# Kernel tuning notes

Measured on AMD Instinct MI355X. Metric: run time of the kernel, lower is better.

## Reference

```python
import jax, jax.numpy as jnp
import numpy as np

FILTER_SIZE = 9
WIN_NUMEL = FILTER_SIZE ** 3  # 729
EPS = 1e-06


def _conv3d_valid(x, w):
    # x: [N,1,D,H,W], w: [1,1,k,k,k]; valid padding, stride 1 (matches F.conv3d padding=0)
    return jax.lax.conv_general_dilated(
        x, w, window_strides=(1, 1, 1), padding='VALID',
        dimension_numbers=('NCDHW', 'OIDHW', 'NCDHW'))


def setup_inputs() -> dict:
    key = jax.random.key(0)
    k1, k2 = jax.random.split(key)
    shape = (1, 1, 160, 160, 160)
    I = jax.random.uniform(k1, shape, dtype=jnp.float32)
    J = jax.random.uniform(k2, shape, dtype=jnp.float32)
    filt = jnp.ones((1, 1, FILTER_SIZE, FILTER_SIZE, FILTER_SIZE), dtype=jnp.float32)
    return {'I': I, 'J': J, 'filt': filt}


def reference(I, J, filt):
    I_sum = _conv3d_valid(I, filt)
    J_sum = _conv3d_valid(J, filt)
    I2_sum = _conv3d_valid(I * I, filt)
    J2_sum = _conv3d_valid(J * J, filt)
    IJ_sum = _conv3d_valid(I * J, filt)

    I_mean = I_sum / WIN_NUMEL
    J_mean = J_sum / WIN_NUMEL

    cross = IJ_sum - I_mean * J_sum - J_mean * I_sum + I_mean * J_mean * WIN_NUMEL
    I_var = I2_sum - 2.0 * I_mean * I_sum + (I_mean ** 2) * WIN_NUMEL
    J_var = J2_sum - 2.0 * J_mean * J_sum + (J_mean ** 2) * WIN_NUMEL

    cc = (cross ** 2) / (I_var * J_var + EPS)
    return 1.0 - jnp.mean(cc)
```

## Files before the change

kernel.cpp:

```cpp
#include <hip/hip_runtime.h>

#define NN 160
#define MM 152
#define TO 16
#define TI 24
#define PSTR 24
#define PCH  (TI*PSTR)
#define XROW 28
#define XCH  (TO*XROW)
#define YROW 20
#define YCH  (TO*YROW)
#define ZC 19
#define PL (ZC+8)
#define KMAX (PL+2)
#define NZ 8
#define NTX 10
#define NTILE 100
#define NBLK (NTILE*8)
#define INV_WIN (1.0f/729.0f)

#define STEP_BARRIER() asm volatile("s_waitcnt lgkmcnt(0)\n\ts_barrier" ::: "memory")

__device__ __forceinline__ float cc_of(const float* s) {
    float cross = fmaf(-s[0] * s[1], INV_WIN, s[4]);
    float iv    = fmaf(-s[0] * s[0], INV_WIN, s[2]);
    float jv    = fmaf(-s[1] * s[1], INV_WIN, s[3]);
    return (cross * cross) / (iv * jv + 1e-6f);
}

__global__ __launch_bounds__(256, 4) void lncc_fused(
    const float* __restrict__ I, const float* __restrict__ J,
    float* __restrict__ partial)
{
    __shared__ float Pld[2][2 * PCH];
    __shared__ float xsb[2][5 * XCH];
    __shared__ float ysb[2][5 * YCH];
    __shared__ float red[4];

    const int tid  = threadIdx.x;
    const int orig = blockIdx.x;
    const int bid  = (orig & 7) * NTILE + (orig >> 3);
    const int tile = bid % NTILE;
    const int zc   = bid / NTILE;
    const int x0 = (tile % NTX) * TO;
    const int y0 = (tile / NTX) * TO;
    const int z0 = zc * ZC;

    const int yl = tid >> 4, xl = tid & 15;
    const bool valid = (x0 + xl < MM) && (y0 + yl < MM);

    const int lrow = tid / 6;
    const int lq   = tid - 6 * lrow;
    const int gy   = min(y0 + lrow, NN - 1);
    const int gx   = min(x0 + lq * 4, NN - 4);
    const size_t pbase = (size_t)gy * NN + gx;

    const int rowX = tid >> 2;
    const int xbX  = (tid & 3) * 4;

    const int eY = tid - 96;
    const int cY = eY >> 4;
    const int xY = eY & 15;

    float4 pI, pJ;
    if (tid < 144) {
        size_t a = (size_t)z0 * (NN * NN) + pbase;
        pI = *(const float4*)(I + a);
        pJ = *(const float4*)(J + a);
    }

    float ring[9][5];
    float sz[5] = {0.f, 0.f, 0.f, 0.f, 0.f};
    float cc_acc = 0.f;

    for (int kb = 0; kb <= KMAX; kb += 9) {
#pragma unroll
        for (int ki = 0; ki < 9; ++ki) {
            const int k = kb + ki;
            if (k > KMAX) continue;

            if (k <= PL - 1 && tid < 144) {
                float* P = &Pld[k & 1][0];
                *(float4*)&P[lrow * PSTR + lq * 4]       = pI;
                *(float4*)&P[PCH + lrow * PSTR + lq * 4] = pJ;
                if (k <= PL - 2) {
                    size_t adr = (size_t)(z0 + k + 1) * (NN * NN) + pbase;
                    pI = *(const float4*)(I + adr);
                    pJ = *(const float4*)(J + adr);
                }
            }

            if (k >= 1 && k <= PL && tid < 96) {
                const int b = (k - 1) & 1;
                const float* P = &Pld[b][0];
                const float4* Ir = (const float4*)&P[rowX * PSTR + xbX];
                const float4* Jr = (const float4*)&P[PCH + rowX * PSTR + xbX];
                float4 i0 = Ir[0], i1 = Ir[1], i2 = Ir[2];
                float4 j0 = Jr[0], j1 = Jr[1], j2 = Jr[2];
                float iv[12], jv[12];
                iv[0]=i0.x; iv[1]=i0.y; iv[2]=i0.z; iv[3]=i0.w;
                iv[4]=i1.x; iv[5]=i1.y; iv[6]=i1.z; iv[7]=i1.w;
                iv[8]=i2.x; iv[9]=i2.y; iv[10]=i2.z; iv[11]=i2.w;
                jv[0]=j0.x; jv[1]=j0.y; jv[2]=j0.z; jv[3]=j0.w;
                jv[4]=j1.x; jv[5]=j1.y; jv[6]=j1.z; jv[7]=j1.w;
                jv[8]=j2.x; jv[9]=j2.y; jv[10]=j2.z; jv[11]=j2.w;
#pragma unroll
                for (int c = 0; c < 5; ++c) {
                    float m[12];
#pragma unroll
                    for (int t = 0; t < 12; ++t) {
                        float av = (c & 1) ? jv[t] : iv[t];
                        float bv = (c < 2) ? 1.0f : ((c == 2) ? iv[t] : jv[t]);
                        m[t] = av * bv;
                    }
                    float s = m[0]+m[1]+m[2]+m[3]+m[4]+m[5]+m[6]+m[7]+m[8];
                    float* W = &xsb[b][c * XCH + rowX];
                    W[xbX * XROW] = s;
#pragma unroll
                    for (int t = 1; t < 4; ++t) {
                        s += m[t + 8] - m[t - 1];
                        W[(xbX + t) * XROW] = s;
                    }
                }
            }

            if (k >= 2 && k <= PL + 1 && tid >= 96 && tid < 176) {
                const int b = (k - 2) & 1;
                const float4* R = (const float4*)&xsb[b][cY * XCH + xY * XROW];
                float4 w0 = R[0], w1 = R[1], w2 = R[2], w3 = R[3], w4 = R[4], w5 = R[5];
                float m[24];
                m[0]=w0.x;  m[1]=w0.y;  m[2]=w0.z;  m[3]=w0.w;
                m[4]=w1.x;  m[5]=w1.y;  m[6]=w1.z;  m[7]=w1.w;
                m[8]=w2.x;  m[9]=w2.y;  m[10]=w2.z; m[11]=w2.w;
                m[12]=w3.x; m[13]=w3.y; m[14]=w3.z; m[15]=w3.w;
                m[16]=w4.x; m[17]=w4.y; m[18]=w4.z; m[19]=w4.w;
                m[20]=w5.x; m[21]=w5.y; m[22]=w5.z; m[23]=w5.w;
                float o[16];
                float s = m[0]+m[1]+m[2]+m[3]+m[4]+m[5]+m[6]+m[7]+m[8];
                o[0] = s;
#pragma unroll
                for (int t = 1; t < 16; ++t) {
                    s += m[t + 8] - m[t - 1];
                    o[t] = s;
                }
                float4* Wv = (float4*)&ysb[b][cY * YCH + xY * YROW];
                float4 oa = {o[0],  o[1],  o[2],  o[3]};
                float4 ob = {o[4],  o[5],  o[6],  o[7]};
                float4 oc = {o[8],  o[9],  o[10], o[11]};
                float4 od = {o[12], o[13], o[14], o[15]};
                Wv[0] = oa; Wv[1] = ob; Wv[2] = oc; Wv[3] = od;
            }

            if (k >= 3) {
                const int b = (k - 3) & 1;
                const int slot  = (ki + 6) % 9;
                const int slot2 = (ki + 7) % 9;
                float v[5];
#pragma unroll
                for (int c = 0; c < 5; ++c) {
                    v[c] = ysb[b][c * YCH + xl * YROW + yl];
                    sz[c] += v[c];
                    ring[slot][c] = v[c];
                }
                if (k >= 11) {
                    cc_acc += valid ? cc_of(sz) : 0.f;
#pragma unroll
                    for (int c = 0; c < 5; ++c) sz[c] -= ring[slot2][c];
                }
            }

            STEP_BARRIER();
        }
    }

    for (int off = 32; off > 0; off >>= 1)
        cc_acc += __shfl_down(cc_acc, off, 64);
    if ((tid & 63) == 0) red[tid >> 6] = cc_acc;
    __syncthreads();
    if (tid == 0) partial[orig] = red[0] + red[1] + red[2] + red[3];
}

__global__ __launch_bounds__(256) void lncc_final(
    const float* __restrict__ partial, float* __restrict__ out)
{
    double s = 0.0;
    for (int i = threadIdx.x; i < NBLK; i += 256)
        s += (double)partial[i];
    for (int off = 32; off > 0; off >>= 1)
        s += __shfl_down(s, off, 64);
    __shared__ double red[4];
    const int lane = threadIdx.x & 63, wid = threadIdx.x >> 6;
    if (lane == 0) red[wid] = s;
    __syncthreads();
    if (threadIdx.x == 0) {
        double tot = red[0] + red[1] + red[2] + red[3];
        out[0] = (float)(1.0 - tot / ((double)MM * MM * MM));
    }
}

extern "C" void kernel_launch(void* const* d_in, const int* in_sizes, int n_in,
                              void* d_out, int out_size, void* d_ws, size_t ws_size,
                              hipStream_t stream) {
    const float* I = (const float*)d_in[0];
    const float* J = (const float*)d_in[1];

    float* partial = (float*)d_ws;

    lncc_fused<<<NBLK, 256, 0, stream>>>(I, J, partial);
    lncc_final<<<1,    256, 0, stream>>>(partial, (float*)d_out);
    (void)in_sizes; (void)n_in; (void)out_size; (void)ws_size;
}
```

Before: 38.67 us.

## Reshape tiles to 8x32 and rebalance warp roles across load, x and y passes

Changes the per-block output tile from 16x16 to 8 wide by 32 tall, which makes the x-direction halo cover an exact 152-wide grid (19 tiles, no invalid x columns) and changes the halo overhead ratio. Reassigns thread roles so that 80 threads do the x-pass, 80 threads load two float4 pairs each, and 80 threads do the y-pass, so that stages no longer sit on overlapping warps and wave-level divergence drops. The cost is a larger y halo (40 rows loaded for 32 outputs) and different LDS strides, which may bring bank conflicts.

```diff
diff --git a/kernel.cpp b/kernel.cpp
--- a/kernel.cpp
+++ b/kernel.cpp
@@ -2,20 +2,21 @@
 
 #define NN 160
 #define MM 152
-#define TO 16
-#define TI 24
-#define PSTR 24
-#define PCH  (TI*PSTR)
-#define XROW 28
-#define XCH  (TO*XROW)
-#define YROW 20
-#define YCH  (TO*YROW)
+#define TOX 8
+#define TOY 32
+#define TIX 16
+#define TIY 40
+#define PS  20
+#define PCH (TIY*PS)
+#define XST 44
+#define XCH (TOX*XST)
+#define YST 36
+#define YCH (TOX*YST)
 #define ZC 19
-#define PL (ZC+8)
-#define KMAX (PL+2)
-#define NZ 8
-#define NTX 10
-#define NTILE 100
+#define PL 27
+#define KMAX 29
+#define NTX 19
+#define NTILE 95
 #define NBLK (NTILE*8)
 #define INV_WIN (1.0f/729.0f)
 
@@ -42,31 +43,34 @@
     const int bid  = (orig & 7) * NTILE + (orig >> 3);
     const int tile = bid % NTILE;
     const int zc   = bid / NTILE;
-    const int x0 = (tile % NTX) * TO;
-    const int y0 = (tile / NTX) * TO;
+    const int x0 = (tile % NTX) * TOX;
+    const int y0 = (tile / NTX) * TOY;
     const int z0 = zc * ZC;
 
-    const int yl = tid >> 4, xl = tid & 15;
-    const bool valid = (x0 + xl < MM) && (y0 + yl < MM);
-
-    const int lrow = tid / 6;
-    const int lq   = tid - 6 * lrow;
-    const int gy   = min(y0 + lrow, NN - 1);
-    const int gx   = min(x0 + lq * 4, NN - 4);
-    const size_t pbase = (size_t)gy * NN + gx;
-
-    const int rowX = tid >> 2;
-    const int xbX  = (tid & 3) * 4;
-
-    const int eY = tid - 96;
-    const int cY = eY >> 4;
-    const int xY = eY & 15;
-
-    float4 pI, pJ;
-    if (tid < 144) {
-        size_t a = (size_t)z0 * (NN * NN) + pbase;
-        pI = *(const float4*)(I + a);
-        pJ = *(const float4*)(J + a);
+    const int yl = tid >> 3, xl = tid & 7;
+    const bool valid = (y0 + yl < MM);
+
+    const int rowX = tid >> 1;
+    const int qX   = tid & 1;
+
+    const int ce = tid - 80;
+    const int r0 = ce >> 2,        q0 = ce & 3;
+    const int r1 = (ce + 80) >> 2, q1 = (ce + 80) & 3;
+    const size_t gb0 = (size_t)min(y0 + r0, NN - 1) * NN + (x0 + q0 * 4);
+    const size_t gb1 = (size_t)min(y0 + r1, NN - 1) * NN + (x0 + q1 * 4);
+
+    const int eY  = tid - 176;
+    const int cY  = eY >> 4;
+    const int xY  = (eY >> 1) & 7;
+    const int yhY = eY & 1;
+
+    float4 pI0, pJ0, pI1, pJ1;
+    if (tid >= 80 && tid < 160) {
+        const size_t zb = (size_t)z0 * (NN * NN);
+        pI0 = *(const float4*)(I + zb + gb0);
+        pJ0 = *(const float4*)(J + zb + gb0);
+        pI1 = *(const float4*)(I + zb + gb1);
+        pJ1 = *(const float4*)(J + zb + gb1);
     }
 
     float ring[9][5];
@@ -79,22 +83,26 @@
             const int k = kb + ki;
             if (k > KMAX) continue;
 
-            if (k <= PL - 1 && tid < 144) {
+            if (k <= PL - 1 && tid >= 80 && tid < 160) {
                 float* P = &Pld[k & 1][0];
-                *(float4*)&P[lrow * PSTR + lq * 4]       = pI;
-                *(float4*)&P[PCH + lrow * PSTR + lq * 4] = pJ;
+                *(float4*)&P[r0 * PS + q0 * 4]       = pI0;
+                *(float4*)&P[PCH + r0 * PS + q0 * 4] = pJ0;
+                *(float4*)&P[r1 * PS + q1 * 4]       = pI1;
+                *(float4*)&P[PCH + r1 * PS + q1 * 4] = pJ1;
                 if (k <= PL - 2) {
-                    size_t adr = (size_t)(z0 + k + 1) * (NN * NN) + pbase;
-                    pI = *(const float4*)(I + adr);
-                    pJ = *(const float4*)(J + adr);
-                }
-            }
-
-            if (k >= 1 && k <= PL && tid < 96) {
+                    const size_t zb = (size_t)(z0 + k + 1) * (NN * NN);
+                    pI0 = *(const float4*)(I + zb + gb0);
+                    pJ0 = *(const float4*)(J + zb + gb0);
+                    pI1 = *(const float4*)(I + zb + gb1);
+                    pJ1 = *(const float4*)(J + zb + gb1);
+                }
+            }
+
+            if (k >= 1 && k <= PL && tid < 80) {
                 const int b = (k - 1) & 1;
                 const float* P = &Pld[b][0];
-                const float4* Ir = (const float4*)&P[rowX * PSTR + xbX];
-                const float4* Jr = (const float4*)&P[PCH + rowX * PSTR + xbX];
+                const float4* Ir = (const float4*)&P[rowX * PS + qX * 4];
+                const float4* Jr = (const float4*)&P[PCH + rowX * PS + qX * 4];
                 float4 i0 = Ir[0], i1 = Ir[1], i2 = Ir[2];
                 float4 j0 = Jr[0], j1 = Jr[1], j2 = Jr[2];
                 float iv[12], jv[12];
@@ -115,19 +123,21 @@
                     }
                     float s = m[0]+m[1]+m[2]+m[3]+m[4]+m[5]+m[6]+m[7]+m[8];
                     float* W = &xsb[b][c * XCH + rowX];
-                    W[xbX * XROW] = s;
+                    W[(qX * 4) * XST] = s;
 #pragma unroll
                     for (int t = 1; t < 4; ++t) {
                         s += m[t + 8] - m[t - 1];
-                        W[(xbX + t) * XROW] = s;
+                        W[(qX * 4 + t) * XST] = s;
                     }
                 }
             }
 
-            if (k >= 2 && k <= PL + 1 && tid >= 96 && tid < 176) {
+            if (k >= 2 && k <= PL + 1 && tid >= 176) {
                 const int b = (k - 2) & 1;
-                const float4* R = (const float4*)&xsb[b][cY * XCH + xY * XROW];
-                float4 w0 = R[0], w1 = R[1], w2 = R[2], w3 = R[3], w4 = R[4], w5 = R[5];
+                const float* xb = &xsb[b][cY * XCH + xY * XST + yhY * 16];
+                float4 w0 = ((const float4*)xb)[0], w1 = ((const float4*)xb)[1],
+                       w2 = ((const float4*)xb)[2], w3 = ((const float4*)xb)[3],
+                       w4 = ((const float4*)xb)[4], w5 = ((const float4*)xb)[5];
                 float m[24];
                 m[0]=w0.x;  m[1]=w0.y;  m[2]=w0.z;  m[3]=w0.w;
                 m[4]=w1.x;  m[5]=w1.y;  m[6]=w1.z;  m[7]=w1.w;
@@ -143,12 +153,13 @@
                     s += m[t + 8] - m[t - 1];
                     o[t] = s;
                 }
-                float4* Wv = (float4*)&ysb[b][cY * YCH + xY * YROW];
+                float* yb = &ysb[b][cY * YCH + xY * YST + yhY * 16];
                 float4 oa = {o[0],  o[1],  o[2],  o[3]};
                 float4 ob = {o[4],  o[5],  o[6],  o[7]};
                 float4 oc = {o[8],  o[9],  o[10], o[11]};
                 float4 od = {o[12], o[13], o[14], o[15]};
-                Wv[0] = oa; Wv[1] = ob; Wv[2] = oc; Wv[3] = od;
+                ((float4*)yb)[0] = oa; ((float4*)yb)[1] = ob;
+                ((float4*)yb)[2] = oc; ((float4*)yb)[3] = od;
             }
 
             if (k >= 3) {
@@ -158,7 +169,7 @@
                 float v[5];
 #pragma unroll
                 for (int c = 0; c < 5; ++c) {
-                    v[c] = ysb[b][c * YCH + xl * YROW + yl];
+                    v[c] = ysb[b][c * YCH + xl * YST + yl];
                     sz[c] += v[c];
                     ring[slot][c] = v[c];
                 }
```

Result: faster. 34.91 us, median of 3 (-9.7%).
